# Performance work log

Hardware: AMD Instinct MI355X
Metric: run time of the kernel (lower is better)

Reference implementation:

```python
import jax, jax.numpy as jnp
import numpy as np

BATCH, SEQ, DIM = 2, 2048, 1024
HEADS, HEAD_DIM = 16, 64
K_NEI = 64
SCALE = 1.0 / float(np.sqrt(HEAD_DIM))


def _cantor_routes(seq_len: int, k: int, depth: int = 8) -> np.ndarray:
    """Replicates _build_positional_routes: Cantor coords + topk smallest |ci-cj|."""
    pos = np.arange(seq_len, dtype=np.float64)
    x = pos / max(1, seq_len - 1)
    x = np.clip(x, 1e-6, 1.0 - 1e-6)
    val = np.zeros_like(x)
    factor = 0.5
    for _ in range(depth):
        xs = x * 3.0
        digit = np.floor(xs)
        x = xs - digit
        val = val + (digit == 2.0).astype(np.float64) * factor
        factor *= 0.5
    val = np.clip(val, 0.0, 1.0)
    dist = np.abs(val[:, None] - val[None, :])  # [S, S]
    routes = np.argsort(dist, axis=1, kind='stable')[:, :k]  # smallest-k neighbors
    return routes.astype(np.int32)


def setup_inputs() -> dict:
    key = jax.random.key(0)
    kx, kw1, kb1, kw2, kb2 = jax.random.split(key, 5)
    x = jax.random.normal(kx, (BATCH, SEQ, DIM), dtype=jnp.float32)
    qkv_w = jax.random.normal(kw1, (3 * DIM, DIM), dtype=jnp.float32) * 0.02
    qkv_b = jax.random.normal(kb1, (3 * DIM,), dtype=jnp.float32) * 0.02
    out_w = jax.random.normal(kw2, (DIM, DIM), dtype=jnp.float32) * 0.02
    out_b = jax.random.normal(kb2, (DIM,), dtype=jnp.float32) * 0.02
    routes = jnp.asarray(_cantor_routes(SEQ, K_NEI))  # [S, K] int32
    return {"x": x, "routes": routes, "qkv_w": qkv_w, "qkv_b": qkv_b,
            "out_w": out_w, "out_b": out_b}


def reference(x, routes, qkv_w, qkv_b, out_w, out_b):
    B, S, _ = x.shape
    # QKV projection (torch Linear: x @ W.T + b)
    qkv = x @ qkv_w.T + qkv_b                          # [B, S, 3*DIM]
    qkv = qkv.reshape(B, S, 3, HEADS, HEAD_DIM).transpose(2, 0, 3, 1, 4)
    q, k, v = qkv[0], qkv[1], qkv[2]                   # each [B, H, S, D]
    # Gather K/V along precomputed Cantor routes: [B, H, S, K, D]
    k_g = jnp.take(k, routes, axis=2)
    v_g = jnp.take(v, routes, axis=2)
    scores = jnp.einsum('bhqd,bhqkd->bhqk', q, k_g) * SCALE
    attn = jax.nn.softmax(scores, axis=-1)             # [B, H, S, K]
    out = jnp.einsum('bhqk,bhqkd->bhqd', attn, v_g)    # [B, H, S, D]
    out = out.transpose(0, 2, 1, 3).reshape(B, S, DIM)
    return out @ out_w.T + out_b
```

## Files before the change

### kernel.cpp

```cpp
#include <hip/hip_runtime.h>
#include <math.h>

#define BATCH    2
#define SEQ      2048
#define DIM      1024
#define HEADS    16
#define HEAD_DIM 64
#define K_NEI    64
#define QKV_DIM  3072
#define MROWS    (BATCH * SEQ)
#define ATT_SCALE 0.125f
#define CHUNK    16
#define MAXCH    2048

typedef _Float16 half8  __attribute__((ext_vector_type(8)));
typedef _Float16 half4  __attribute__((ext_vector_type(4)));
typedef _Float16 half2t __attribute__((ext_vector_type(2)));
typedef float    floatx4 __attribute__((ext_vector_type(4)));

__device__ inline void async_copy16(const void* g, void* l) {
  __builtin_amdgcn_global_load_lds(
      (const __attribute__((address_space(1))) unsigned int*)g,
      (__attribute__((address_space(3))) unsigned int*)l, 16, 0, 0);
}

__global__ __launch_bounds__(256)
void cast3(const float* __restrict__ a, int na4,
           const float* __restrict__ b, int nb4,
           const float* __restrict__ c, int nc4,
           _Float16* __restrict__ oa, _Float16* __restrict__ ob,
           _Float16* __restrict__ oc) {
  const int total = na4 + nb4 + nc4;
  for (int i = blockIdx.x * blockDim.x + threadIdx.x; i < total;
       i += gridDim.x * blockDim.x) {
    const float* src; _Float16* dst; int idx;
    if (i < na4)            { src = a; dst = oa; idx = i; }
    else if (i < na4 + nb4) { src = b; dst = ob; idx = i - na4; }
    else                    { src = c; dst = oc; idx = i - na4 - nb4; }
    float4 v = *(const float4*)(src + (size_t)idx * 4);
    half4 o;
    o[0] = (_Float16)v.x; o[1] = (_Float16)v.y;
    o[2] = (_Float16)v.z; o[3] = (_Float16)v.w;
    *(half4*)(dst + (size_t)idx * 4) = o;
  }
}

template<int BM, int BN, bool HALF_OUT>
__global__ __launch_bounds__(256)
void gemm_bt_f16(const _Float16* __restrict__ A, const _Float16* __restrict__ B,
                 const float* __restrict__ bias, void* __restrict__ Cv,
                 int M, int N, int K) {
  constexpr int FI = BM / 32;
  constexpr int FJ = BN / 32;
  constexpr int CA = BM / 64;
  constexpr int CB = BN / 64;
  __shared__ _Float16 As[2 * BM * 32];
  __shared__ _Float16 Bs[2 * BN * 32];

  const int tid  = threadIdx.x;
  const int lane = tid & 63;
  const int w    = tid >> 6;
  const int wr   = w >> 1;
  const int wc   = w & 1;
  const int bm   = blockIdx.y * BM;
  const int bn   = blockIdx.x * BN;

  const int srow = w * 16 + (lane >> 2);
  const int scol = (lane & 3) * 8;
  const _Float16* ga = A + (size_t)(bm + srow) * K + scol;
  const _Float16* gb = B + (size_t)(bn + srow) * K + scol;

  const int frow = lane & 15;
  const int fk   = (lane >> 4) * 8;

  floatx4 acc[FI][FJ] = {};

  for (int k0 = 0; k0 < K; k0 += 64) {
#pragma unroll
    for (int sub = 0; sub < 2; sub++) {
      const int kk = k0 + sub * 32;
#pragma unroll
      for (int i = 0; i < CA; i++)
        async_copy16(ga + (size_t)(i * 64) * K + kk,
                     As + sub * BM * 32 + w * 512 + i * 2048);
#pragma unroll
      for (int i = 0; i < CB; i++)
        async_copy16(gb + (size_t)(i * 64) * K + kk,
                     Bs + sub * BN * 32 + w * 512 + i * 2048);
    }
    __syncthreads();

#pragma unroll
    for (int sub = 0; sub < 2; sub++) {
      half8 af[FI], bf[FJ];
#pragma unroll
      for (int i = 0; i < FI; i++)
        af[i] = *(const half8*)&As[sub * BM * 32 + (wr * (BM / 2) + i * 16 + frow) * 32 + fk];
#pragma unroll
      for (int j = 0; j < FJ; j++)
        bf[j] = *(const half8*)&Bs[sub * BN * 32 + (wc * (BN / 2) + j * 16 + frow) * 32 + fk];
#pragma unroll
      for (int i = 0; i < FI; i++)
#pragma unroll
        for (int j = 0; j < FJ; j++) {
          if (HALF_OUT)
            acc[i][j] = __builtin_amdgcn_mfma_f32_16x16x32_f16(bf[j], af[i], acc[i][j], 0, 0, 0);
          else
            acc[i][j] = __builtin_amdgcn_mfma_f32_16x16x32_f16(af[i], bf[j], acc[i][j], 0, 0, 0);
        }
    }
    __syncthreads();
  }

  if (HALF_OUT) {
    _Float16* C = (_Float16*)Cv;
    const int mloc = lane & 15;
    const int nloc = (lane >> 4) * 4;
#pragma unroll
    for (int j = 0; j < FJ; j++) {
      const int gcol = bn + wc * (BN / 2) + j * 16 + nloc;
      float4 bj = *(const float4*)(bias + gcol);
#pragma unroll
      for (int i = 0; i < FI; i++) {
        const int grow = bm + wr * (BM / 2) + i * 16 + mloc;
        half4 hv;
        hv[0] = (_Float16)(acc[i][j][0] + bj.x);
        hv[1] = (_Float16)(acc[i][j][1] + bj.y);
        hv[2] = (_Float16)(acc[i][j][2] + bj.z);
        hv[3] = (_Float16)(acc[i][j][3] + bj.w);
        *(half4*)(C + (size_t)grow * N + gcol) = hv;
      }
    }
  } else {
    float* C = (float*)Cv;
    const int crow = (lane >> 4) * 4;
    const int ccol = lane & 15;
#pragma unroll
    for (int j = 0; j < FJ; j++) {
      const int gcol = bn + wc * (BN / 2) + j * 16 + ccol;
      const float bj = bias[gcol];
#pragma unroll
      for (int i = 0; i < FI; i++) {
        const int grow = bm + wr * (BM / 2) + i * 16 + crow;
        float* cp = C + (size_t)grow * N + gcol;
#pragma unroll
        for (int r = 0; r < 4; r++)
          cp[(size_t)r * N] = acc[i][j][r] + bj;
      }
    }
  }
}

__global__ __launch_bounds__(64)
void group_map(const int* __restrict__ routes, int* __restrict__ gq) {
  const int q = blockIdx.x * 64 + threadIdx.x;
  if (q >= SEQ) return;
  const int lead = routes[q * K_NEI];
  bool same = (lead >= 0) && (lead < SEQ);
  if (same && lead != q) {
    const int4* a = (const int4*)(routes + q * K_NEI);
    const int4* b = (const int4*)(routes + lead * K_NEI);
#pragma unroll
    for (int t = 0; t < 16; t++) {
      int4 x = a[t], y = b[t];
      same = same && (x.x == y.x) && (x.y == y.y) && (x.z == y.z) && (x.w == y.w);
    }
  }
  gq[q] = same ? lead : q;
}

__global__ __launch_bounds__(256)
void group_emit(const int* __restrict__ gq, int* __restrict__ gmem,
                int* __restrict__ chunks, int* __restrict__ meta) {
  __shared__ int cnt[SEQ];
  __shared__ int base[SEQ];
  __shared__ int warpsum[8];
  __shared__ int nch_sm;
  const int tid = threadIdx.x;

  for (int i = tid; i < SEQ; i += 256) cnt[i] = 0;
  if (tid == 0) nch_sm = 0;
  __syncthreads();

  for (int q = tid; q < SEQ; q += 256) atomicAdd(&cnt[gq[q]], 1);
  __syncthreads();

  int local[8];
  int s = 0;
#pragma unroll
  for (int k = 0; k < 8; k++) { local[k] = s; s += cnt[tid * 8 + k]; }
  const int lane = tid & 63, wv = tid >> 6;
  int sc = s;
#pragma unroll
  for (int off = 1; off < 64; off <<= 1) {
    int t2 = __shfl_up(sc, off);
    if (lane >= off) sc += t2;
  }
  if (lane == 63) warpsum[wv] = sc;
  __syncthreads();
  int wvoff = 0;
  for (int k = 0; k < wv; k++) wvoff += warpsum[k];
  const int thrbase = wvoff + sc - s;
#pragma unroll
  for (int k = 0; k < 8; k++) base[tid * 8 + k] = thrbase + local[k];
  __syncthreads();

  for (int gg = tid; gg < SEQ; gg += 256) {
    const int c = cnt[gg];
    if (c > 0) {
      const int nchk = (c + CHUNK - 1) / CHUNK;
      const int slot = atomicAdd(&nch_sm, nchk);
      for (int k2 = 0; k2 < nchk; k2++) {
        const int sidx = slot + k2;
        if (sidx < MAXCH) {
          const int len = min(CHUNK, c - k2 * CHUNK);
          chunks[2 * sidx]     = gg;
          chunks[2 * sidx + 1] = (base[gg] + k2 * CHUNK) | (len << 16);
        }
      }
    }
  }
  __syncthreads();
  if (tid == 0) meta[0] = min(nch_sm, MAXCH);

  for (int q = tid; q < SEQ; q += 256) {
    const int slot = atomicAdd(&base[gq[q]], 1);
    gmem[slot] = q;
  }
}

__global__ __launch_bounds__(128)
void attn_mfma(const _Float16* __restrict__ qkv, const int* __restrict__ routes,
               const int* __restrict__ gmem, const int* __restrict__ chunks,
               const int* __restrict__ meta, _Float16* __restrict__ ao) {
  __shared__ _Float16 lds[2][9216];

  const int tid  = threadIdx.x;
  const int w    = tid >> 6;
  const int lane = tid & 63;
  const int g    = lane >> 4;
  const int c    = lane & 15;

  _Float16* Ks = &lds[w][0];
  _Float16* Vs = &lds[w][4096];
  _Float16* Ps = &lds[w][8192];

  const int nch    = meta[0];
  const int njobs  = nch * 32;
  const int nwaves = gridDim.x * 2;

  const int c8   = (lane & 7) ^ ((lane >> 3) & 7);
  const int rsub = lane >> 3;

  for (int job = blockIdx.x * 2 + w; job < njobs; job += nwaves) {
    const int ch = job >> 5;
    const int bh = job & 31;
    const int h  = bh & 15;
    const int b  = bh >> 4;

    const int gid   = chunks[2 * ch];
    const int mpack = chunks[2 * ch + 1];
    const int mbase = mpack & 0xFFFF;
    const int mlen  = mpack >> 16;
    const size_t rowb = (size_t)b * SEQ;

    const int rt_l = routes[gid * K_NEI + lane];
    const int qm_l = gmem[mbase + min(c, mlen - 1)];

#pragma unroll
    for (int k = 0; k < 8; k++) {
      const int row = __shfl(rt_l, 8 * k + rsub);
      const _Float16* kp = qkv + (rowb + row) * QKV_DIM + DIM + h * HEAD_DIM + c8 * 8;
      async_copy16(kp,       Ks + k * 512);
      async_copy16(kp + DIM, Vs + k * 512);
    }

    const _Float16* qrow = qkv + (rowb + qm_l) * QKV_DIM + h * HEAD_DIM + g * 8;
    const half8 qf0 = *(const half8*)(qrow);
    const half8 qf1 = *(const half8*)(qrow + 32);

    asm volatile("s_waitcnt vmcnt(0)" ::: "memory");

    floatx4 st[4] = {};
    const half8 qf[2] = { qf0, qf1 };
#pragma unroll
    for (int s2 = 0; s2 < 2; s2++) {
#pragma unroll
      for (int m = 0; m < 4; m++) {
        const int r = m * 16 + c;
        const half8 kf =
            *(const half8*)&Ks[r * 64 + ((((s2 << 2) + g) ^ (c & 7)) << 3)];
        st[m] = __builtin_amdgcn_mfma_f32_16x16x32_f16(kf, qf[s2], st[m], 0, 0, 0);
      }
    }

    float mx = st[0][0];
#pragma unroll
    for (int m = 0; m < 4; m++)
#pragma unroll
      for (int r = 0; r < 4; r++) mx = fmaxf(mx, st[m][r]);
    mx = fmaxf(mx, __shfl_xor(mx, 16));
    mx = fmaxf(mx, __shfl_xor(mx, 32));

    float p[16];
    float sum = 0.f;
#pragma unroll
    for (int m = 0; m < 4; m++)
#pragma unroll
      for (int r = 0; r < 4; r++) {
        const float e = __expf((st[m][r] - mx) * ATT_SCALE);
        p[m * 4 + r] = e;
        sum += e;
      }
    sum += __shfl_xor(sum, 16);
    sum += __shfl_xor(sum, 32);
    const float inv = 1.0f / sum;

#pragma unroll
    for (int m = 0; m < 4; m++) {
      half4 ph;
      ph[0] = (_Float16)(p[m * 4 + 0] * inv);
      ph[1] = (_Float16)(p[m * 4 + 1] * inv);
      ph[2] = (_Float16)(p[m * 4 + 2] * inv);
      ph[3] = (_Float16)(p[m * 4 + 3] * inv);
      const int idx = c * 64 + (((2 * m + (g >> 1)) ^ (c & 7)) << 3) + ((g & 1) << 2);
      *(half4*)&Ps[idx] = ph;
    }
    asm volatile("s_waitcnt lgkmcnt(0)" ::: "memory");

    half8 pf[2];
#pragma unroll
    for (int s2 = 0; s2 < 2; s2++)
      pf[s2] = *(const half8*)&Ps[c * 64 + ((((s2 << 2) + g) ^ (c & 7)) << 3)];

    floatx4 oa[4] = {};
#pragma unroll
    for (int n = 0; n < 4; n++) {
      const int dtop = 2 * n + (c >> 3);
#pragma unroll
      for (int s2 = 0; s2 < 2; s2++) {
        half8 vf;
#pragma unroll
        for (int j = 0; j < 8; j++) {
          const int rr = s2 * 32 + g * 8 + j;
          vf[j] = Vs[rr * 64 + ((dtop ^ j) << 3) + (c & 7)];
        }
        oa[n] = __builtin_amdgcn_mfma_f32_16x16x32_f16(pf[s2], vf, oa[n], 0, 0, 0);
      }
    }

#pragma unroll
    for (int r = 0; r < 4; r++) {
      const int i = g * 4 + r;
      const int qrow_i = __shfl(qm_l, i);
      if (i < mlen) {
        _Float16* op = ao + (rowb + qrow_i) * DIM + h * HEAD_DIM + c;
#pragma unroll
        for (int n = 0; n < 4; n++) op[n * 16] = (_Float16)oa[n][r];
      }
    }
  }
}

extern "C" void kernel_launch(void* const* d_in, const int* in_sizes, int n_in,
                              void* d_out, int out_size, void* d_ws, size_t ws_size,
                              hipStream_t stream) {
  const float* x      = (const float*)d_in[0];
  const int*   routes = (const int*)  d_in[1];
  const float* qkv_w  = (const float*)d_in[2];
  const float* qkv_b  = (const float*)d_in[3];
  const float* out_w  = (const float*)d_in[4];
  const float* out_b  = (const float*)d_in[5];
  float* out = (float*)d_out;

  _Float16* qkvh = (_Float16*)d_ws;
  _Float16* aoh  = qkvh + (size_t)MROWS * QKV_DIM;
  _Float16* xh   = aoh  + (size_t)MROWS * DIM;
  _Float16* wh   = xh   + (size_t)MROWS * DIM;
  _Float16* owh  = wh   + (size_t)QKV_DIM * DIM;

  char* scr   = (char*)d_out + (size_t)out_size - 65536;
  int* gq     = (int*)scr;
  int* gmem   = gq + SEQ;
  int* chunks = gmem + SEQ;
  int* meta   = chunks + 2 * MAXCH;

  group_map <<<SEQ / 64, 64, 0, stream>>>(routes, gq);
  group_emit<<<1, 256, 0, stream>>>(gq, gmem, chunks, meta);

  cast3<<<1024, 256, 0, stream>>>(x, MROWS * DIM / 4,
                                  qkv_w, QKV_DIM * DIM / 4,
                                  out_w, DIM * DIM / 4,
                                  xh, wh, owh);

  {
    dim3 g(QKV_DIM / 128, MROWS / 128);
    gemm_bt_f16<128, 128, true><<<g, 256, 0, stream>>>(xh, wh, qkv_b, qkvh,
                                                       MROWS, QKV_DIM, DIM);
  }

  attn_mfma<<<4096, 128, 0, stream>>>(qkvh, routes, gmem, chunks, meta, aoh);

  {
    dim3 g(DIM / 128, MROWS / 64);
    gemm_bt_f16<64, 128, false><<<g, 256, 0, stream>>>(aoh, owh, out_b, out,
                                                       MROWS, DIM, DIM);
  }
}
```

Before: 177.3 us.

## Load K fragments directly from global into registers, staging only V in LDS

The attention kernel stops staging gathered K rows through LDS. Each lane now loads its K MFMA fragments straight from global memory into registers, and only V goes through async global-to-LDS copies. The vmcnt wait is pushed back to just before the PV stage, so the V copies overlap with QK^T and softmax. LDS per block shrinks and launch_bounds asks for 3 blocks per CU, trading higher register pressure and less coalesced K loads for more occupancy and overlap.

```diff
diff --git a/kernel.cpp b/kernel.cpp
--- a/kernel.cpp
+++ b/kernel.cpp
@@ -229,11 +229,11 @@
   }
 }
 
-__global__ __launch_bounds__(128)
+__global__ __launch_bounds__(128, 3)
 void attn_mfma(const _Float16* __restrict__ qkv, const int* __restrict__ routes,
                const int* __restrict__ gmem, const int* __restrict__ chunks,
                const int* __restrict__ meta, _Float16* __restrict__ ao) {
-  __shared__ _Float16 lds[2][9216];
+  __shared__ _Float16 lds[2][5120];
 
   const int tid  = threadIdx.x;
   const int w    = tid >> 6;
@@ -241,9 +241,8 @@
   const int g    = lane >> 4;
   const int c    = lane & 15;
 
-  _Float16* Ks = &lds[w][0];
-  _Float16* Vs = &lds[w][4096];
-  _Float16* Ps = &lds[w][8192];
+  _Float16* Vs = &lds[w][0];
+  _Float16* Ps = &lds[w][4096];
 
   const int nch    = meta[0];
   const int njobs  = nch * 32;
@@ -267,32 +266,39 @@
     const int rt_l = routes[gid * K_NEI + lane];
     const int qm_l = gmem[mbase + min(c, mlen - 1)];
 
+    int krow[4];
+#pragma unroll
+    for (int m = 0; m < 4; m++) krow[m] = __shfl(rt_l, m * 16 + c);
+
+    asm volatile("s_waitcnt lgkmcnt(0)" ::: "memory");
+    __builtin_amdgcn_sched_barrier(0);
+
 #pragma unroll
     for (int k = 0; k < 8; k++) {
       const int row = __shfl(rt_l, 8 * k + rsub);
-      const _Float16* kp = qkv + (rowb + row) * QKV_DIM + DIM + h * HEAD_DIM + c8 * 8;
-      async_copy16(kp,       Ks + k * 512);
-      async_copy16(kp + DIM, Vs + k * 512);
+      const _Float16* vp = qkv + (rowb + row) * QKV_DIM + 2 * DIM + h * HEAD_DIM + c8 * 8;
+      async_copy16(vp, Vs + k * 512);
     }
 
     const _Float16* qrow = qkv + (rowb + qm_l) * QKV_DIM + h * HEAD_DIM + g * 8;
     const half8 qf0 = *(const half8*)(qrow);
     const half8 qf1 = *(const half8*)(qrow + 32);
-
-    asm volatile("s_waitcnt vmcnt(0)" ::: "memory");
+    const half8 qf[2] = { qf0, qf1 };
+
+    half8 kf[2][4];
+#pragma unroll
+    for (int s2 = 0; s2 < 2; s2++)
+#pragma unroll
+      for (int m = 0; m < 4; m++)
+        kf[s2][m] = *(const half8*)(qkv + (rowb + krow[m]) * QKV_DIM + DIM
+                                    + h * HEAD_DIM + s2 * 32 + g * 8);
 
     floatx4 st[4] = {};
-    const half8 qf[2] = { qf0, qf1 };
-#pragma unroll
-    for (int s2 = 0; s2 < 2; s2++) {
-#pragma unroll
-      for (int m = 0; m < 4; m++) {
-        const int r = m * 16 + c;
-        const half8 kf =
-            *(const half8*)&Ks[r * 64 + ((((s2 << 2) + g) ^ (c & 7)) << 3)];
-        st[m] = __builtin_amdgcn_mfma_f32_16x16x32_f16(kf, qf[s2], st[m], 0, 0, 0);
-      }
-    }
+#pragma unroll
+    for (int s2 = 0; s2 < 2; s2++)
+#pragma unroll
+      for (int m = 0; m < 4; m++)
+        st[m] = __builtin_amdgcn_mfma_f32_16x16x32_f16(kf[s2][m], qf[s2], st[m], 0, 0, 0);
 
     float mx = st[0][0];
 #pragma unroll
@@ -326,7 +332,9 @@
       const int idx = c * 64 + (((2 * m + (g >> 1)) ^ (c & 7)) << 3) + ((g & 1) << 2);
       *(half4*)&Ps[idx] = ph;
     }
-    asm volatile("s_waitcnt lgkmcnt(0)" ::: "memory");
+
+    asm volatile("s_waitcnt vmcnt(0) lgkmcnt(0)" ::: "memory");
+    __builtin_amdgcn_sched_barrier(0);
 
     half8 pf[2];
 #pragma unroll
```

New measurement: 178.1 us. No clear change (+0.5%).

## Process four heads per block with cooperative K/V gather and coalesced output

Applied to the files above, without the earlier changes.

The attention kernel now assigns one (chunk, batch, 4-head group) job to a 256-thread block, with each wave handling one head. K/V rows for all four heads are gathered cooperatively as contiguous 512-byte segments into shared LDS. The per-head output is staged through LDS so each query row is written with 16-byte vector stores instead of scattered 2-byte writes. This adds block-level barriers and more LDS per block, which may lower occupancy and makes the waves wait on each other.

```diff
diff --git a/kernel.cpp b/kernel.cpp
--- a/kernel.cpp
+++ b/kernel.cpp
@@ -229,11 +229,16 @@
   }
 }
 
-__global__ __launch_bounds__(128)
-void attn_mfma(const _Float16* __restrict__ qkv, const int* __restrict__ routes,
-               const int* __restrict__ gmem, const int* __restrict__ chunks,
-               const int* __restrict__ meta, _Float16* __restrict__ ao) {
-  __shared__ _Float16 lds[2][9216];
+__global__ __launch_bounds__(256, 2)
+void attn_mfma4(const _Float16* __restrict__ qkv, const int* __restrict__ routes,
+                const int* __restrict__ gmem, const int* __restrict__ chunks,
+                const int* __restrict__ meta, _Float16* __restrict__ ao) {
+  __shared__ _Float16 Ks[64 * 256];
+  __shared__ _Float16 Vs[64 * 256];
+  __shared__ union {
+    _Float16 P[4][1024];
+    _Float16 O[16 * 264];
+  } u;
 
   const int tid  = threadIdx.x;
   const int w    = tid >> 6;
@@ -241,58 +246,54 @@
   const int g    = lane >> 4;
   const int c    = lane & 15;
 
-  _Float16* Ks = &lds[w][0];
-  _Float16* Vs = &lds[w][4096];
-  _Float16* Ps = &lds[w][8192];
-
-  const int nch    = meta[0];
-  const int njobs  = nch * 32;
-  const int nwaves = gridDim.x * 2;
-
-  const int c8   = (lane & 7) ^ ((lane >> 3) & 7);
-  const int rsub = lane >> 3;
-
-  for (int job = blockIdx.x * 2 + w; job < njobs; job += nwaves) {
-    const int ch = job >> 5;
-    const int bh = job & 31;
-    const int h  = bh & 15;
-    const int b  = bh >> 4;
+  const int nch   = meta[0];
+  const int njobs = nch * BATCH * 4;
+
+  const int slot  = tid & 31;
+  const int rbase = tid >> 5;
+
+  for (int job = blockIdx.x; job < njobs; job += gridDim.x) {
+    const int ch = job >> 3;
+    const int b  = (job >> 2) & 1;
+    const int hg = job & 3;
+    const int h  = hg * 4 + w;
 
     const int gid   = chunks[2 * ch];
     const int mpack = chunks[2 * ch + 1];
     const int mbase = mpack & 0xFFFF;
     const int mlen  = mpack >> 16;
     const size_t rowb = (size_t)b * SEQ;
-
-    const int rt_l = routes[gid * K_NEI + lane];
-    const int qm_l = gmem[mbase + min(c, mlen - 1)];
-
-#pragma unroll
-    for (int k = 0; k < 8; k++) {
-      const int row = __shfl(rt_l, 8 * k + rsub);
-      const _Float16* kp = qkv + (rowb + row) * QKV_DIM + DIM + h * HEAD_DIM + c8 * 8;
-      async_copy16(kp,       Ks + k * 512);
-      async_copy16(kp + DIM, Vs + k * 512);
-    }
-
-    const _Float16* qrow = qkv + (rowb + qm_l) * QKV_DIM + h * HEAD_DIM + g * 8;
+    const int hb = hg * 256;
+
+#pragma unroll
+    for (int i = 0; i < 8; i++) {
+      const int row = i * 8 + rbase;
+      const int nr  = routes[gid * K_NEI + row];
+      const int sg  = slot ^ (row & 7);
+      const _Float16* kp = qkv + (rowb + nr) * QKV_DIM + DIM + hb + sg * 8;
+      async_copy16(kp,       Ks + (i * 256 + tid) * 8);
+      async_copy16(kp + DIM, Vs + (i * 256 + tid) * 8);
+    }
+
+    const int qm = gmem[mbase + min(c, mlen - 1)];
+    const _Float16* qrow = qkv + (rowb + qm) * QKV_DIM + h * HEAD_DIM + g * 8;
     const half8 qf0 = *(const half8*)(qrow);
     const half8 qf1 = *(const half8*)(qrow + 32);
+    const half8 qf[2] = { qf0, qf1 };
 
     asm volatile("s_waitcnt vmcnt(0)" ::: "memory");
+    __syncthreads();
 
     floatx4 st[4] = {};
-    const half8 qf[2] = { qf0, qf1 };
-#pragma unroll
-    for (int s2 = 0; s2 < 2; s2++) {
+#pragma unroll
+    for (int s2 = 0; s2 < 2; s2++)
 #pragma unroll
       for (int m = 0; m < 4; m++) {
-        const int r = m * 16 + c;
-        const half8 kf =
-            *(const half8*)&Ks[r * 64 + ((((s2 << 2) + g) ^ (c & 7)) << 3)];
+        const int row = m * 16 + c;
+        const half8 kf = *(const half8*)
+            &Ks[row * 256 + w * 64 + ((((s2 << 2) + g) ^ (c & 7)) << 3)];
         st[m] = __builtin_amdgcn_mfma_f32_16x16x32_f16(kf, qf[s2], st[m], 0, 0, 0);
       }
-    }
 
     float mx = st[0][0];
 #pragma unroll
@@ -324,16 +325,17 @@
       ph[2] = (_Float16)(p[m * 4 + 2] * inv);
       ph[3] = (_Float16)(p[m * 4 + 3] * inv);
       const int idx = c * 64 + (((2 * m + (g >> 1)) ^ (c & 7)) << 3) + ((g & 1) << 2);
-      *(half4*)&Ps[idx] = ph;
+      *(half4*)&u.P[w][idx] = ph;
     }
     asm volatile("s_waitcnt lgkmcnt(0)" ::: "memory");
+    __builtin_amdgcn_sched_barrier(0);
 
     half8 pf[2];
 #pragma unroll
     for (int s2 = 0; s2 < 2; s2++)
-      pf[s2] = *(const half8*)&Ps[c * 64 + ((((s2 << 2) + g) ^ (c & 7)) << 3)];
-
-    floatx4 oa[4] = {};
+      pf[s2] = *(const half8*)&u.P[w][c * 64 + ((((s2 << 2) + g) ^ (c & 7)) << 3)];
+
+    floatx4 oacc[4] = {};
 #pragma unroll
     for (int n = 0; n < 4; n++) {
       const int dtop = 2 * n + (c >> 3);
@@ -343,22 +345,33 @@
 #pragma unroll
         for (int j = 0; j < 8; j++) {
           const int rr = s2 * 32 + g * 8 + j;
-          vf[j] = Vs[rr * 64 + ((dtop ^ j) << 3) + (c & 7)];
+          vf[j] = Vs[rr * 256 + w * 64 + ((dtop ^ j) << 3) + (c & 7)];
         }
-        oa[n] = __builtin_amdgcn_mfma_f32_16x16x32_f16(pf[s2], vf, oa[n], 0, 0, 0);
-      }
-    }
-
-#pragma unroll
-    for (int r = 0; r < 4; r++) {
-      const int i = g * 4 + r;
-      const int qrow_i = __shfl(qm_l, i);
+        oacc[n] = __builtin_amdgcn_mfma_f32_16x16x32_f16(pf[s2], vf, oacc[n], 0, 0, 0);
+      }
+    }
+
+    __syncthreads();
+
+#pragma unroll
+    for (int n = 0; n < 4; n++)
+#pragma unroll
+      for (int r = 0; r < 4; r++)
+        u.O[(g * 4 + r) * 264 + w * 64 + n * 16 + c] = (_Float16)oacc[n][r];
+    __syncthreads();
+
+    {
+      const int i    = tid >> 4;
+      const int part = tid & 15;
       if (i < mlen) {
-        _Float16* op = ao + (rowb + qrow_i) * DIM + h * HEAD_DIM + c;
-#pragma unroll
-        for (int n = 0; n < 4; n++) op[n * 16] = (_Float16)oa[n][r];
-      }
-    }
+        const int qr = gmem[mbase + i];
+        _Float16* op = ao + (rowb + qr) * DIM + hg * 256 + part * 16;
+        const _Float16* sp = &u.O[i * 264 + part * 16];
+        *(half8*)op       = *(const half8*)sp;
+        *(half8*)(op + 8) = *(const half8*)(sp + 8);
+      }
+    }
+    __syncthreads();
   }
 }
 
@@ -399,7 +412,7 @@
                                                        MROWS, QKV_DIM, DIM);
   }
 
-  attn_mfma<<<4096, 128, 0, stream>>>(qkvh, routes, gmem, chunks, meta, aoh);
+  attn_mfma4<<<2048, 256, 0, stream>>>(qkvh, routes, gmem, chunks, meta, aoh);
 
   {
     dim3 g(DIM / 128, MROWS / 64);
```

After: 180.3 us. About the same (+1.7%).
